# Kernel optimization log

Hardware: AMD Instinct MI355X
Metric: run time of the kernel (lower is better)

The kernel has to match this reference:

```python
import jax, jax.numpy as jnp
import numpy as np

H = 8
D = 64  # head_dim = node_dim // num_heads = 512 // 8
NODE = 512
EPS = 1e-5


def setup_inputs() -> dict:
    key = jax.random.key(0)
    ks = jax.random.split(key, 8)
    S, IN = 4096, 1024
    return {
        "protT5_emb": jax.random.normal(ks[0], (S, IN), jnp.float32),
        "contact_matrix": jax.random.uniform(ks[1], (S, S), jnp.float32),
        "Wq": jax.random.normal(ks[2], (NODE, IN), jnp.float32) * 0.02,
        "bq": jnp.zeros((NODE,), jnp.float32),
        "Wk": jax.random.normal(ks[3], (NODE, IN), jnp.float32) * 0.02,
        "bk": jnp.zeros((NODE,), jnp.float32),
        "Wv": jax.random.normal(ks[4], (NODE, IN), jnp.float32) * 0.02,
        "bv": jnp.zeros((NODE,), jnp.float32),
        "Wc": jnp.ones((1, H, 1, 1), jnp.float32),
        "Wo": jax.random.normal(ks[5], (NODE, NODE), jnp.float32) * 0.02,
        "bo": jnp.zeros((NODE,), jnp.float32),
        "gamma": jnp.ones((NODE,), jnp.float32),
        "beta": jnp.zeros((NODE,), jnp.float32),
    }


def reference(protT5_emb, contact_matrix, Wq, bq, Wk, bk, Wv, bv, Wc, Wo, bo, gamma, beta):
    S = protT5_emb.shape[0]
    # QKV projections -> [H, S, D]
    Q = (protT5_emb @ Wq.T + bq).reshape(S, H, D).transpose(1, 0, 2)
    K = (protT5_emb @ Wk.T + bk).reshape(S, H, D).transpose(1, 0, 2)
    V = (protT5_emb @ Wv.T + bv).reshape(S, H, D).transpose(1, 0, 2)
    # raw scores [H, S, S]
    attn_raw = jnp.einsum('hsd,htd->hst', Q, K) / jnp.sqrt(jnp.float32(D))
    # multiplicative contact mask, per-head learnable scale
    contact_mask = contact_matrix[None, :, :] * Wc.reshape(H, 1, 1)
    attn_weight = jax.nn.softmax(attn_raw * contact_mask, axis=-1)
    attn_output = jnp.einsum('hst,htd->hsd', attn_weight, V)  # [H, S, D]
    # FAITHFUL to torch: transpose(0,1).view(S,-1) on [1,H,S,D] flattens in
    # (head, seq, dim) order -> scrambled [S, H*D] reshape, not head concat.
    attn_output = attn_output.reshape(S, H * D)
    aug = attn_output @ Wo.T + bo
    x = aug + protT5_emb[:, :NODE]
    mu = jnp.mean(x, axis=-1, keepdims=True)
    var = jnp.mean((x - mu) ** 2, axis=-1, keepdims=True)
    return (x - mu) * jax.lax.rsqrt(var + EPS) * gamma + beta
```

## Files before the change

kernel.cpp:

```cpp
#include <hip/hip_runtime.h>
#include <stdint.h>

#define SEQ 4096
#define INDIM 1024
#define NODEDIM 512
#define NH 8
#define HD 64
#define LSTR 72

typedef __bf16 bf16x8 __attribute__((ext_vector_type(8)));
typedef float f32x4 __attribute__((ext_vector_type(4)));

#define GLOAD_LDS(gp, lp) \
    __builtin_amdgcn_global_load_lds( \
        (const __attribute__((address_space(1))) void*)(gp), \
        (__attribute__((address_space(3))) void*)(lp), 16, 0, 0)

__device__ __forceinline__ unsigned short f2bf(float f) {
    union { float f; uint32_t u; } v; v.f = f;
    uint32_t u = v.u;
    uint32_t r = (u + 0x7fffu + ((u >> 16) & 1u)) >> 16;
    return (unsigned short)r;
}

__device__ __forceinline__ float fast_exp2(float x) {
    float r;
    asm volatile("v_exp_f32 %0, %1" : "=v"(r) : "v"(x));
    return r;
}

__global__ __launch_bounds__(256) void cvt_all(const float* __restrict__ emb,
                                               const float* __restrict__ Wq,
                                               const float* __restrict__ Wk,
                                               const float* __restrict__ Wv,
                                               const float* __restrict__ Wo,
                                               unsigned short* __restrict__ demb,
                                               unsigned short* __restrict__ dwqkv,
                                               unsigned short* __restrict__ dwo) {
    int b = blockIdx.x;
    const float* src;
    unsigned short* dst;
    int off;
    if (b < 4096)      { src = emb; dst = demb;            off = b; }
    else if (b < 4608) { src = Wq;  dst = dwqkv;           off = b - 4096; }
    else if (b < 5120) { src = Wk;  dst = dwqkv + 524288;  off = b - 4608; }
    else if (b < 5632) { src = Wv;  dst = dwqkv + 1048576; off = b - 5120; }
    else               { src = Wo;  dst = dwo;             off = b - 5632; }
    int i = (off * 256 + threadIdx.x) * 4;
    float4 v = *(const float4*)(src + i);
    ushort4 o;
    o.x = f2bf(v.x); o.y = f2bf(v.y); o.z = f2bf(v.z); o.w = f2bf(v.w);
    *(ushort4*)(dst + i) = o;
}

__global__ __launch_bounds__(256) void qkv_gemm(const unsigned short* __restrict__ A,
                                                const unsigned short* __restrict__ B,
                                                const float* __restrict__ bq,
                                                const float* __restrict__ bk,
                                                const float* __restrict__ bv,
                                                unsigned short* __restrict__ Qo,
                                                unsigned short* __restrict__ Ko,
                                                unsigned short* __restrict__ VTo) {
    __shared__ unsigned short As[128 * 32];
    __shared__ unsigned short Bs[128 * 32];
    __shared__ unsigned short Ts[128 * 40];
    const int tid = threadIdx.x;
    const int lane = tid & 63, wave = tid >> 6;
    const int wm = wave >> 1, wn = wave & 1;
    const int quad = lane >> 4, l16 = lane & 15;
    const int m0 = blockIdx.x * 128;
    const int n0 = blockIdx.y * 128;

    const int srow = tid >> 2, sqq = tid & 3;

    f32x4 acc[4][4] = {};

    for (int k0 = 0; k0 < INDIM; k0 += 32) {
        __syncthreads();
        for (int i = 0; i < 2; ++i) {
            int row = srow + 64 * i;
            GLOAD_LDS(A + (size_t)(m0 + row) * INDIM + k0 + sqq * 8, &As[row * 32 + sqq * 8]);
            GLOAD_LDS(B + (size_t)(n0 + row) * INDIM + k0 + sqq * 8, &Bs[row * 32 + sqq * 8]);
        }
        __syncthreads();
        bf16x8 af[4], bf[4];
        for (int mi = 0; mi < 4; ++mi)
            af[mi] = *(const bf16x8*)&As[(wm * 64 + mi * 16 + l16) * 32 + quad * 8];
        for (int ni = 0; ni < 4; ++ni)
            bf[ni] = *(const bf16x8*)&Bs[(wn * 64 + ni * 16 + l16) * 32 + quad * 8];
        for (int mi = 0; mi < 4; ++mi)
            for (int ni = 0; ni < 4; ++ni)
                acc[mi][ni] = __builtin_amdgcn_mfma_f32_16x16x32_bf16(af[mi], bf[ni], acc[mi][ni], 0, 0, 0);
    }

    if (blockIdx.y < 8) {
        unsigned short* outp = (blockIdx.y < 4) ? Qo : Ko;
        const float* biasp = (blockIdx.y < 4) ? bq : bk;
        for (int mi = 0; mi < 4; ++mi)
            for (int ni = 0; ni < 4; ++ni)
                for (int r = 0; r < 4; ++r) {
                    int s = m0 + wm * 64 + mi * 16 + quad * 4 + r;
                    int n = n0 + wn * 64 + ni * 16 + l16;
                    int h = (n >> 6) & 7;
                    int dd = n & 63;
                    float v = acc[mi][ni][r] + biasp[n & 511];
                    outp[((size_t)h * SEQ + s) * HD + dd] = f2bf(v);
                }
    } else {
        for (int chunk = 0; chunk < 4; ++chunk) {
            const int cwm = chunk >> 1;
            const int milo = (chunk & 1) * 2;
            __syncthreads();
            if (wm == cwm) {
                for (int mi2 = 0; mi2 < 2; ++mi2) {
                    int mi = milo + mi2;
                    for (int ni = 0; ni < 4; ++ni) {
                        int ddf = wn * 64 + ni * 16 + l16;
                        float bias = bv[(n0 + ddf) & 511];
                        for (int r = 0; r < 4; ++r) {
                            int sl = mi2 * 16 + quad * 4 + r;
                            Ts[ddf * 40 + sl] = f2bf(acc[mi][ni][r] + bias);
                        }
                    }
                }
            }
            __syncthreads();
            for (int pass = 0; pass < 2; ++pass) {
                int c = pass * 256 + tid;
                int row = c >> 2, part = c & 3;
                int nfull = n0 + row;
                int h = (nfull >> 6) & 7, dd = nfull & 63;
                *(bf16x8*)(VTo + ((size_t)h * HD + dd) * SEQ + m0 + chunk * 32 + part * 8) =
                    *(const bf16x8*)&Ts[row * 40 + part * 8];
            }
        }
    }
}

__global__ __launch_bounds__(256, 4) void attn_kernel(const unsigned short* __restrict__ Q,
                                                      const unsigned short* __restrict__ K,
                                                      const unsigned short* __restrict__ VT,
                                                      const float* __restrict__ CM,
                                                      const float* __restrict__ Wc,
                                                      float* __restrict__ O0,
                                                      float* __restrict__ O1,
                                                      float* __restrict__ l0,
                                                      float* __restrict__ l1) {
    __shared__ unsigned short QPs[64 * LSTR];
    __shared__ unsigned short Ks[64 * LSTR];
    __shared__ unsigned short Vs[64 * LSTR];
    const int tid = threadIdx.x;
    const int lane = tid & 63, wave = tid >> 6;
    const int quad = lane >> 4, l16 = lane & 15;
    const int h = blockIdx.y;
    const int q0 = blockIdx.x * 64;
    const int split = blockIdx.z;
    float* __restrict__ Op = split ? O1 : O0;
    float* __restrict__ lp = split ? l1 : l0;
    const float wch = Wc[h] * 0.125f * 1.44269504f;

    const int srow0 = tid >> 3, spart = tid & 7;
    const int srow1 = (tid + 256) >> 3;

    {
        bf16x8 v0 = *(const bf16x8*)(Q + ((size_t)h * SEQ + q0 + srow0) * HD + spart * 8);
        bf16x8 v1 = *(const bf16x8*)(Q + ((size_t)h * SEQ + q0 + srow1) * HD + spart * 8);
        for (int j = 0; j < 8; ++j) {
            v0[j] = (__bf16)((float)v0[j] * wch);
            v1[j] = (__bf16)((float)v1[j] * wch);
        }
        *(bf16x8*)&QPs[srow0 * LSTR + spart * 8] = v0;
        *(bf16x8*)&QPs[srow1 * LSTR + spart * 8] = v1;
    }

    const int tbeg = split * (SEQ / 2);
    const int tend = tbeg + SEQ / 2;

    const unsigned short* kp0 = K + ((size_t)h * SEQ + tbeg + srow0) * HD + spart * 8;
    const unsigned short* kp1 = K + ((size_t)h * SEQ + tbeg + srow1) * HD + spart * 8;
    const unsigned short* vp0 = VT + ((size_t)h * HD + srow0) * SEQ + tbeg + spart * 8;
    const unsigned short* vp1 = VT + ((size_t)h * HD + srow1) * SEQ + tbeg + spart * 8;
    bf16x8 kr0 = *(const bf16x8*)kp0;
    bf16x8 kr1 = *(const bf16x8*)kp1;
    bf16x8 vr0 = *(const bf16x8*)vp0;
    bf16x8 vr1 = *(const bf16x8*)vp1;

    const float* cmbase = CM + (size_t)(q0 + wave * 16 + quad * 4) * SEQ + l16;
    float cmv[4][4];
    for (int r = 0; r < 4; ++r)
        for (int nt = 0; nt < 4; ++nt)
            cmv[r][nt] = cmbase[(size_t)r * SEQ + tbeg + nt * 16];

    __syncthreads();
    bf16x8 a0 = *(const bf16x8*)&QPs[(wave * 16 + l16) * LSTR + quad * 8];
    bf16x8 a1 = *(const bf16x8*)&QPs[(wave * 16 + l16) * LSTR + 32 + quad * 8];

    f32x4 O[4] = {};
    float l_part[4] = {0.f, 0.f, 0.f, 0.f};

    for (int t0 = tbeg; t0 < tend; t0 += 64) {
        __syncthreads();
        *(bf16x8*)&Ks[srow0 * LSTR + spart * 8] = kr0;
        *(bf16x8*)&Ks[srow1 * LSTR + spart * 8] = kr1;
        *(bf16x8*)&Vs[srow0 * LSTR + spart * 8] = vr0;
        *(bf16x8*)&Vs[srow1 * LSTR + spart * 8] = vr1;
        __syncthreads();

        float cmn[4][4];
        if (t0 + 64 < tend) {
            kr0 = *(const bf16x8*)(kp0 + (size_t)(t0 + 64 - tbeg) * HD);
            kr1 = *(const bf16x8*)(kp1 + (size_t)(t0 + 64 - tbeg) * HD);
            vr0 = *(const bf16x8*)(vp0 + (t0 + 64 - tbeg));
            vr1 = *(const bf16x8*)(vp1 + (t0 + 64 - tbeg));
            for (int r = 0; r < 4; ++r)
                for (int nt = 0; nt < 4; ++nt)
                    cmn[r][nt] = cmbase[(size_t)r * SEQ + t0 + 64 + nt * 16];
        }

        f32x4 sc[4];
        for (int nt = 0; nt < 4; ++nt) {
            bf16x8 b0 = *(const bf16x8*)&Ks[(nt * 16 + l16) * LSTR + quad * 8];
            bf16x8 b1 = *(const bf16x8*)&Ks[(nt * 16 + l16) * LSTR + 32 + quad * 8];
            f32x4 z = {0.f, 0.f, 0.f, 0.f};
            z = __builtin_amdgcn_mfma_f32_16x16x32_bf16(a0, b0, z, 0, 0, 0);
            z = __builtin_amdgcn_mfma_f32_16x16x32_bf16(a1, b1, z, 0, 0, 0);
            sc[nt] = z;
        }

        for (int r = 0; r < 4; ++r) {
            for (int nt = 0; nt < 4; ++nt) {
                float pv = fast_exp2(sc[nt][r] * cmv[r][nt]);
                l_part[r] += pv;
                union { float f; uint32_t u; } pu; pu.f = pv;
                QPs[(wave * 16 + quad * 4 + r) * LSTR + nt * 16 + l16] =
                    (unsigned short)(pu.u >> 16);
            }
        }

        for (int r = 0; r < 4; ++r)
            for (int nt = 0; nt < 4; ++nt)
                cmv[r][nt] = cmn[r][nt];

        asm volatile("s_waitcnt lgkmcnt(0)" ::: "memory");

        bf16x8 pa0 = *(const bf16x8*)&QPs[(wave * 16 + l16) * LSTR + quad * 8];
        bf16x8 pa1 = *(const bf16x8*)&QPs[(wave * 16 + l16) * LSTR + 32 + quad * 8];
        for (int nt = 0; nt < 4; ++nt) {
            bf16x8 vb0 = *(const bf16x8*)&Vs[(nt * 16 + l16) * LSTR + quad * 8];
            bf16x8 vb1 = *(const bf16x8*)&Vs[(nt * 16 + l16) * LSTR + 32 + quad * 8];
            f32x4 o = O[nt];
            o = __builtin_amdgcn_mfma_f32_16x16x32_bf16(pa0, vb0, o, 0, 0, 0);
            o = __builtin_amdgcn_mfma_f32_16x16x32_bf16(pa1, vb1, o, 0, 0, 0);
            O[nt] = o;
        }
    }

    for (int r = 0; r < 4; ++r) {
        float s = l_part[r];
        for (int off = 1; off < 16; off <<= 1) s += __shfl_xor(s, off);
        l_part[r] = s;
    }
    if (l16 == 0)
        for (int r = 0; r < 4; ++r)
            lp[(size_t)h * SEQ + q0 + wave * 16 + quad * 4 + r] = l_part[r];
    for (int nt = 0; nt < 4; ++nt)
        for (int r = 0; r < 4; ++r) {
            int sg = q0 + wave * 16 + quad * 4 + r;
            Op[((size_t)h * SEQ + sg) * HD + nt * 16 + l16] = O[nt][r];
        }
}

__global__ __launch_bounds__(256) void combine_kernel(const float* __restrict__ O0,
                                                      const float* __restrict__ O1,
                                                      const float* __restrict__ l0,
                                                      const float* __restrict__ l1,
                                                      unsigned short* __restrict__ AO) {
    int idx = blockIdx.x * 256 + threadIdx.x;
    int e = idx * 4;
    int row = e >> 6;
    float4 a = *(const float4*)(O0 + e);
    float4 b = *(const float4*)(O1 + e);
    float linv = 1.f / (l0[row] + l1[row]);
    ushort4 o;
    o.x = f2bf((a.x + b.x) * linv);
    o.y = f2bf((a.y + b.y) * linv);
    o.z = f2bf((a.z + b.z) * linv);
    o.w = f2bf((a.w + b.w) * linv);
    *(ushort4*)(AO + e) = o;
}

__global__ __launch_bounds__(256) void out_gemm(const unsigned short* __restrict__ A,
                                                const unsigned short* __restrict__ B,
                                                const float* __restrict__ bo,
                                                const float* __restrict__ emb,
                                                float* __restrict__ X) {
    __shared__ unsigned short As[64 * 32];
    __shared__ unsigned short Bs[128 * 32];
    const int tid = threadIdx.x;
    const int lane = tid & 63, wave = tid >> 6;
    const int quad = lane >> 4, l16 = lane & 15;
    const int m0 = blockIdx.x * 64;
    const int n0 = blockIdx.y * 128;

    const int srow = tid >> 2, sqq = tid & 3;

    f32x4 acc[8] = {};

    for (int k0 = 0; k0 < NODEDIM; k0 += 32) {
        __syncthreads();
        GLOAD_LDS(A + (size_t)(m0 + srow) * NODEDIM + k0 + sqq * 8, &As[srow * 32 + sqq * 8]);
        for (int i = 0; i < 2; ++i) {
            int row = srow + 64 * i;
            GLOAD_LDS(B + (size_t)(n0 + row) * NODEDIM + k0 + sqq * 8, &Bs[row * 32 + sqq * 8]);
        }
        __syncthreads();
        bf16x8 af = *(const bf16x8*)&As[(wave * 16 + l16) * 32 + quad * 8];
        for (int ni = 0; ni < 8; ++ni) {
            bf16x8 bf = *(const bf16x8*)&Bs[(ni * 16 + l16) * 32 + quad * 8];
            acc[ni] = __builtin_amdgcn_mfma_f32_16x16x32_bf16(af, bf, acc[ni], 0, 0, 0);
        }
    }

    for (int ni = 0; ni < 8; ++ni)
        for (int r = 0; r < 4; ++r) {
            int s = m0 + wave * 16 + quad * 4 + r;
            int n = n0 + ni * 16 + l16;
            float v = acc[ni][r] + bo[n] + emb[(size_t)s * INDIM + n];
            X[(size_t)s * NODEDIM + n] = v;
        }
}

__global__ __launch_bounds__(256) void ln_kernel(const float* __restrict__ X,
                                                 const float* __restrict__ gamma,
                                                 const float* __restrict__ beta,
                                                 float* __restrict__ out) {
    const int s = blockIdx.x;
    const int n = threadIdx.x * 2;
    float2 v = *(const float2*)&X[(size_t)s * NODEDIM + n];
    float sum = v.x + v.y;
    float sq = v.x * v.x + v.y * v.y;
    for (int off = 32; off > 0; off >>= 1) {
        sum += __shfl_down(sum, off);
        sq += __shfl_down(sq, off);
    }
    __shared__ float ssum[4], ssq[4];
    const int wave = threadIdx.x >> 6, lane = threadIdx.x & 63;
    if (lane == 0) { ssum[wave] = sum; ssq[wave] = sq; }
    __syncthreads();
    float tsum = ssum[0] + ssum[1] + ssum[2] + ssum[3];
    float tsq = ssq[0] + ssq[1] + ssq[2] + ssq[3];
    float mu = tsum * (1.f / 512.f);
    float var = tsq * (1.f / 512.f) - mu * mu;
    float rstd = rsqrtf(var + 1e-5f);
    float2 g = *(const float2*)&gamma[n];
    float2 b = *(const float2*)&beta[n];
    float2 o;
    o.x = (v.x - mu) * rstd * g.x + b.x;
    o.y = (v.y - mu) * rstd * g.y + b.y;
    *(float2*)&out[(size_t)s * NODEDIM + n] = o;
}

extern "C" void kernel_launch(void* const* d_in, const int* in_sizes, int n_in,
                              void* d_out, int out_size, void* d_ws, size_t ws_size,
                              hipStream_t stream) {
    const float* emb = (const float*)d_in[0];
    const float* cm  = (const float*)d_in[1];
    const float* Wq  = (const float*)d_in[2];
    const float* bq  = (const float*)d_in[3];
    const float* Wk  = (const float*)d_in[4];
    const float* bk  = (const float*)d_in[5];
    const float* Wv  = (const float*)d_in[6];
    const float* bv  = (const float*)d_in[7];
    const float* Wc  = (const float*)d_in[8];
    const float* Wo  = (const float*)d_in[9];
    const float* bo  = (const float*)d_in[10];
    const float* gamma = (const float*)d_in[11];
    const float* beta  = (const float*)d_in[12];
    float* out = (float*)d_out;

    unsigned short* ws = (unsigned short*)d_ws;
    unsigned short* emb_bf  = ws;
    unsigned short* wqkv_bf = emb_bf + 4194304;
    unsigned short* wo_bf   = wqkv_bf + 1572864;
    unsigned short* Qb  = wo_bf + 262144;
    unsigned short* Kb  = Qb + 2097152;
    unsigned short* VTb = Kb + 2097152;
    unsigned short* AOb = VTb + 2097152;
    float* X = (float*)(AOb + 2097152);
    float* O0 = (float*)emb_bf;
    float* O1 = X;
    float* l0 = (float*)wqkv_bf;
    float* l1 = l0 + NH * SEQ;

    cvt_all<<<5888, 256, 0, stream>>>(emb, Wq, Wk, Wv, Wo, emb_bf, wqkv_bf, wo_bf);

    qkv_gemm<<<dim3(32, 12), 256, 0, stream>>>(emb_bf, wqkv_bf, bq, bk, bv, Qb, Kb, VTb);
    attn_kernel<<<dim3(64, 8, 2), 256, 0, stream>>>(Qb, Kb, VTb, cm, Wc, O0, O1, l0, l1);
    combine_kernel<<<2048, 256, 0, stream>>>(O0, O1, l0, l1, AOb);
    out_gemm<<<dim3(64, 4), 256, 0, stream>>>(AOb, wo_bf, bo, emb, X);
    ln_kernel<<<4096, 256, 0, stream>>>(X, gamma, beta, out);
}
```

Measured before the change: 260.6 us.

## Fuse fp32-to-bf16 conversion into QKV and output GEMM tile loads

Removes the separate cvt_all pass. The QKV and output GEMMs now read fp32 inputs and weights directly and convert them to bf16 while staging into LDS. The QKV GEMM moves to a 128x64 per-head tile (768 blocks instead of 384), and the attention kernel loads its contact-mask values at the top of each iteration instead of prefetching them one step ahead. This saves one kernel launch and the bf16 round trip through memory, at the cost of twice the fp32 read bytes per GEMM tile, redundant conversion work across blocks, and synchronous loads in place of async LDS loads.

```diff
diff --git a/kernel.cpp b/kernel.cpp
--- a/kernel.cpp
+++ b/kernel.cpp
@@ -29,32 +29,20 @@
     return r;
 }
 
-__global__ __launch_bounds__(256) void cvt_all(const float* __restrict__ emb,
-                                               const float* __restrict__ Wq,
-                                               const float* __restrict__ Wk,
-                                               const float* __restrict__ Wv,
-                                               const float* __restrict__ Wo,
-                                               unsigned short* __restrict__ demb,
-                                               unsigned short* __restrict__ dwqkv,
-                                               unsigned short* __restrict__ dwo) {
-    int b = blockIdx.x;
-    const float* src;
-    unsigned short* dst;
-    int off;
-    if (b < 4096)      { src = emb; dst = demb;            off = b; }
-    else if (b < 4608) { src = Wq;  dst = dwqkv;           off = b - 4096; }
-    else if (b < 5120) { src = Wk;  dst = dwqkv + 524288;  off = b - 4608; }
-    else if (b < 5632) { src = Wv;  dst = dwqkv + 1048576; off = b - 5120; }
-    else               { src = Wo;  dst = dwo;             off = b - 5632; }
-    int i = (off * 256 + threadIdx.x) * 4;
-    float4 v = *(const float4*)(src + i);
-    ushort4 o;
-    o.x = f2bf(v.x); o.y = f2bf(v.y); o.z = f2bf(v.z); o.w = f2bf(v.w);
-    *(ushort4*)(dst + i) = o;
-}
-
-__global__ __launch_bounds__(256) void qkv_gemm(const unsigned short* __restrict__ A,
-                                                const unsigned short* __restrict__ B,
+__device__ __forceinline__ void cvt8(const float* __restrict__ p, unsigned short* dst) {
+    float4 u = *(const float4*)p;
+    float4 w = *(const float4*)(p + 4);
+    ushort4 a, b;
+    a.x = f2bf(u.x); a.y = f2bf(u.y); a.z = f2bf(u.z); a.w = f2bf(u.w);
+    b.x = f2bf(w.x); b.y = f2bf(w.y); b.z = f2bf(w.z); b.w = f2bf(w.w);
+    *(ushort4*)dst = a;
+    *(ushort4*)(dst + 4) = b;
+}
+
+__global__ __launch_bounds__(256) void qkv_gemm(const float* __restrict__ emb,
+                                                const float* __restrict__ Wq,
+                                                const float* __restrict__ Wk,
+                                                const float* __restrict__ Wv,
                                                 const float* __restrict__ bq,
                                                 const float* __restrict__ bk,
                                                 const float* __restrict__ bv,
@@ -62,77 +50,74 @@
                                                 unsigned short* __restrict__ Ko,
                                                 unsigned short* __restrict__ VTo) {
     __shared__ unsigned short As[128 * 32];
-    __shared__ unsigned short Bs[128 * 32];
-    __shared__ unsigned short Ts[128 * 40];
+    __shared__ unsigned short Bs[64 * 32];
+    __shared__ unsigned short Ts[64 * 40];
     const int tid = threadIdx.x;
     const int lane = tid & 63, wave = tid >> 6;
-    const int wm = wave >> 1, wn = wave & 1;
     const int quad = lane >> 4, l16 = lane & 15;
     const int m0 = blockIdx.x * 128;
-    const int n0 = blockIdx.y * 128;
-
-    const int srow = tid >> 2, sqq = tid & 3;
-
-    f32x4 acc[4][4] = {};
+    const int role = blockIdx.y >> 3;
+    const int h = blockIdx.y & 7;
+    const int n0 = h * 64;
+    const float* __restrict__ Wsrc = (role == 0) ? Wq : (role == 1) ? Wk : Wv;
+    const float* __restrict__ bias = (role == 0) ? bq : (role == 1) ? bk : bv;
+
+    f32x4 acc[2][4] = {};
 
     for (int k0 = 0; k0 < INDIM; k0 += 32) {
         __syncthreads();
         for (int i = 0; i < 2; ++i) {
-            int row = srow + 64 * i;
-            GLOAD_LDS(A + (size_t)(m0 + row) * INDIM + k0 + sqq * 8, &As[row * 32 + sqq * 8]);
-            GLOAD_LDS(B + (size_t)(n0 + row) * INDIM + k0 + sqq * 8, &Bs[row * 32 + sqq * 8]);
-        }
-        __syncthreads();
-        bf16x8 af[4], bf[4];
-        for (int mi = 0; mi < 4; ++mi)
-            af[mi] = *(const bf16x8*)&As[(wm * 64 + mi * 16 + l16) * 32 + quad * 8];
+            int c = tid + 256 * i;
+            int row = c >> 2, seg = c & 3;
+            unsigned short tmp[8];
+            cvt8(emb + (size_t)(m0 + row) * INDIM + k0 + seg * 8, tmp);
+            *(bf16x8*)&As[row * 32 + seg * 8] = *(bf16x8*)tmp;
+        }
+        {
+            int row = tid >> 2, seg = tid & 3;
+            unsigned short tmp[8];
+            cvt8(Wsrc + (size_t)(n0 + row) * INDIM + k0 + seg * 8, tmp);
+            *(bf16x8*)&Bs[row * 32 + seg * 8] = *(bf16x8*)tmp;
+        }
+        __syncthreads();
+        bf16x8 af[2], bf[4];
+        for (int mi = 0; mi < 2; ++mi)
+            af[mi] = *(const bf16x8*)&As[(wave * 32 + mi * 16 + l16) * 32 + quad * 8];
         for (int ni = 0; ni < 4; ++ni)
-            bf[ni] = *(const bf16x8*)&Bs[(wn * 64 + ni * 16 + l16) * 32 + quad * 8];
-        for (int mi = 0; mi < 4; ++mi)
+            bf[ni] = *(const bf16x8*)&Bs[(ni * 16 + l16) * 32 + quad * 8];
+        for (int mi = 0; mi < 2; ++mi)
             for (int ni = 0; ni < 4; ++ni)
                 acc[mi][ni] = __builtin_amdgcn_mfma_f32_16x16x32_bf16(af[mi], bf[ni], acc[mi][ni], 0, 0, 0);
     }
 
-    if (blockIdx.y < 8) {
-        unsigned short* outp = (blockIdx.y < 4) ? Qo : Ko;
-        const float* biasp = (blockIdx.y < 4) ? bq : bk;
-        for (int mi = 0; mi < 4; ++mi)
+    if (role < 2) {
+        unsigned short* outp = (role == 0) ? Qo : Ko;
+        for (int mi = 0; mi < 2; ++mi)
             for (int ni = 0; ni < 4; ++ni)
                 for (int r = 0; r < 4; ++r) {
-                    int s = m0 + wm * 64 + mi * 16 + quad * 4 + r;
-                    int n = n0 + wn * 64 + ni * 16 + l16;
-                    int h = (n >> 6) & 7;
-                    int dd = n & 63;
-                    float v = acc[mi][ni][r] + biasp[n & 511];
+                    int s = m0 + wave * 32 + mi * 16 + quad * 4 + r;
+                    int dd = ni * 16 + l16;
+                    float v = acc[mi][ni][r] + bias[n0 + dd];
                     outp[((size_t)h * SEQ + s) * HD + dd] = f2bf(v);
                 }
     } else {
         for (int chunk = 0; chunk < 4; ++chunk) {
-            const int cwm = chunk >> 1;
-            const int milo = (chunk & 1) * 2;
             __syncthreads();
-            if (wm == cwm) {
-                for (int mi2 = 0; mi2 < 2; ++mi2) {
-                    int mi = milo + mi2;
+            if (wave == chunk) {
+                for (int mi = 0; mi < 2; ++mi)
                     for (int ni = 0; ni < 4; ++ni) {
-                        int ddf = wn * 64 + ni * 16 + l16;
-                        float bias = bv[(n0 + ddf) & 511];
+                        int ddf = ni * 16 + l16;
+                        float bv_ = bias[n0 + ddf];
                         for (int r = 0; r < 4; ++r) {
-                            int sl = mi2 * 16 + quad * 4 + r;
-                            Ts[ddf * 40 + sl] = f2bf(acc[mi][ni][r] + bias);
+                            int sl = mi * 16 + quad * 4 + r;
+                            Ts[ddf * 40 + sl] = f2bf(acc[mi][ni][r] + bv_);
                         }
                     }
-                }
             }
             __syncthreads();
-            for (int pass = 0; pass < 2; ++pass) {
-                int c = pass * 256 + tid;
-                int row = c >> 2, part = c & 3;
-                int nfull = n0 + row;
-                int h = (nfull >> 6) & 7, dd = nfull & 63;
-                *(bf16x8*)(VTo + ((size_t)h * HD + dd) * SEQ + m0 + chunk * 32 + part * 8) =
-                    *(const bf16x8*)&Ts[row * 40 + part * 8];
-            }
+            int row = tid >> 2, part = tid & 3;
+            *(bf16x8*)(VTo + ((size_t)h * HD + row) * SEQ + m0 + chunk * 32 + part * 8) =
+                *(const bf16x8*)&Ts[row * 40 + part * 8];
         }
     }
 }
@@ -185,20 +170,20 @@
     bf16x8 vr0 = *(const bf16x8*)vp0;
     bf16x8 vr1 = *(const bf16x8*)vp1;
 
-    const float* cmbase = CM + (size_t)(q0 + wave * 16 + quad * 4) * SEQ + l16;
-    float cmv[4][4];
-    for (int r = 0; r < 4; ++r)
-        for (int nt = 0; nt < 4; ++nt)
-            cmv[r][nt] = cmbase[(size_t)r * SEQ + tbeg + nt * 16];
-
     __syncthreads();
     bf16x8 a0 = *(const bf16x8*)&QPs[(wave * 16 + l16) * LSTR + quad * 8];
     bf16x8 a1 = *(const bf16x8*)&QPs[(wave * 16 + l16) * LSTR + 32 + quad * 8];
 
     f32x4 O[4] = {};
     float l_part[4] = {0.f, 0.f, 0.f, 0.f};
+    const float* cmbase = CM + (size_t)(q0 + wave * 16 + quad * 4) * SEQ + l16;
 
     for (int t0 = tbeg; t0 < tend; t0 += 64) {
+        float cmv[4][4];
+        for (int r = 0; r < 4; ++r)
+            for (int nt = 0; nt < 4; ++nt)
+                cmv[r][nt] = cmbase[(size_t)r * SEQ + t0 + nt * 16];
+
         __syncthreads();
         *(bf16x8*)&Ks[srow0 * LSTR + spart * 8] = kr0;
         *(bf16x8*)&Ks[srow1 * LSTR + spart * 8] = kr1;
@@ -206,15 +191,11 @@
         *(bf16x8*)&Vs[srow1 * LSTR + spart * 8] = vr1;
         __syncthreads();
 
-        float cmn[4][4];
         if (t0 + 64 < tend) {
             kr0 = *(const bf16x8*)(kp0 + (size_t)(t0 + 64 - tbeg) * HD);
             kr1 = *(const bf16x8*)(kp1 + (size_t)(t0 + 64 - tbeg) * HD);
             vr0 = *(const bf16x8*)(vp0 + (t0 + 64 - tbeg));
             vr1 = *(const bf16x8*)(vp1 + (t0 + 64 - tbeg));
-            for (int r = 0; r < 4; ++r)
-                for (int nt = 0; nt < 4; ++nt)
-                    cmn[r][nt] = cmbase[(size_t)r * SEQ + t0 + 64 + nt * 16];
         }
 
         f32x4 sc[4];
@@ -236,10 +217,6 @@
                     (unsigned short)(pu.u >> 16);
             }
         }
-
-        for (int r = 0; r < 4; ++r)
-            for (int nt = 0; nt < 4; ++nt)
-                cmv[r][nt] = cmn[r][nt];
 
         asm volatile("s_waitcnt lgkmcnt(0)" ::: "memory");
 
@@ -290,7 +267,7 @@
 }
 
 __global__ __launch_bounds__(256) void out_gemm(const unsigned short* __restrict__ A,
-                                                const unsigned short* __restrict__ B,
+                                                const float* __restrict__ Wo,
                                                 const float* __restrict__ bo,
                                                 const float* __restrict__ emb,
                                                 float* __restrict__ X) {
@@ -310,8 +287,11 @@
         __syncthreads();
         GLOAD_LDS(A + (size_t)(m0 + srow) * NODEDIM + k0 + sqq * 8, &As[srow * 32 + sqq * 8]);
         for (int i = 0; i < 2; ++i) {
-            int row = srow + 64 * i;
-            GLOAD_LDS(B + (size_t)(n0 + row) * NODEDIM + k0 + sqq * 8, &Bs[row * 32 + sqq * 8]);
+            int c = tid + 256 * i;
+            int row = c >> 2, seg = c & 3;
+            unsigned short tmp[8];
+            cvt8(Wo + (size_t)(n0 + row) * NODEDIM + k0 + seg * 8, tmp);
+            *(bf16x8*)&Bs[row * 32 + seg * 8] = *(bf16x8*)tmp;
         }
         __syncthreads();
         bf16x8 af = *(const bf16x8*)&As[(wave * 16 + l16) * 32 + quad * 8];
@@ -379,24 +359,19 @@
     float* out = (float*)d_out;
 
     unsigned short* ws = (unsigned short*)d_ws;
-    unsigned short* emb_bf  = ws;
-    unsigned short* wqkv_bf = emb_bf + 4194304;
-    unsigned short* wo_bf   = wqkv_bf + 1572864;
-    unsigned short* Qb  = wo_bf + 262144;
+    float* O0 = (float*)ws;
+    float* l0 = (float*)(ws + 4194304);
+    float* l1 = l0 + NH * SEQ;
+    unsigned short* Qb  = ws + 4325376;
     unsigned short* Kb  = Qb + 2097152;
     unsigned short* VTb = Kb + 2097152;
     unsigned short* AOb = VTb + 2097152;
     float* X = (float*)(AOb + 2097152);
-    float* O0 = (float*)emb_bf;
     float* O1 = X;
-    float* l0 = (float*)wqkv_bf;
-    float* l1 = l0 + NH * SEQ;
-
-    cvt_all<<<5888, 256, 0, stream>>>(emb, Wq, Wk, Wv, Wo, emb_bf, wqkv_bf, wo_bf);
-
-    qkv_gemm<<<dim3(32, 12), 256, 0, stream>>>(emb_bf, wqkv_bf, bq, bk, bv, Qb, Kb, VTb);
+
+    qkv_gemm<<<dim3(32, 24), 256, 0, stream>>>(emb, Wq, Wk, Wv, bq, bk, bv, Qb, Kb, VTb);
     attn_kernel<<<dim3(64, 8, 2), 256, 0, stream>>>(Qb, Kb, VTb, cm, Wc, O0, O1, l0, l1);
     combine_kernel<<<2048, 256, 0, stream>>>(O0, O1, l0, l1, AOb);
-    out_gemm<<<dim3(64, 4), 256, 0, stream>>>(AOb, wo_bf, bo, emb, X);
+    out_gemm<<<dim3(64, 4), 256, 0, stream>>>(AOb, Wo, bo, emb, X);
     ln_kernel<<<4096, 256, 0, stream>>>(X, gamma, beta, out);
 }
```

New measurement: 276.6 us. 1.06x slower.

## Double query rows per attention block to reuse K/V tiles across two M-tiles

Applied to the files above, without the earlier changes.

Each attention block now handles 128 query rows instead of 64, and each wave computes two 16-row M-tiles against every K/V tile it stages in LDS. This halves how often K and V are reloaded per query and halves the grid to 512 blocks. The contact-matrix prefetch into registers for the next tile is dropped, so those loads are now issued at the top of each iteration and their latency is no longer hidden by the previous tile's work. Register pressure roughly doubles for the accumulators, which may lower occupancy with only 512 blocks.

```diff
diff --git a/kernel.cpp b/kernel.cpp
--- a/kernel.cpp
+++ b/kernel.cpp
@@ -146,36 +146,32 @@
                                                       float* __restrict__ O1,
                                                       float* __restrict__ l0,
                                                       float* __restrict__ l1) {
-    __shared__ unsigned short QPs[64 * LSTR];
+    __shared__ unsigned short QPs[128 * LSTR];
     __shared__ unsigned short Ks[64 * LSTR];
     __shared__ unsigned short Vs[64 * LSTR];
     const int tid = threadIdx.x;
     const int lane = tid & 63, wave = tid >> 6;
     const int quad = lane >> 4, l16 = lane & 15;
     const int h = blockIdx.y;
-    const int q0 = blockIdx.x * 64;
+    const int q0 = blockIdx.x * 128;
     const int split = blockIdx.z;
     float* __restrict__ Op = split ? O1 : O0;
     float* __restrict__ lp = split ? l1 : l0;
     const float wch = Wc[h] * 0.125f * 1.44269504f;
 
+    for (int i = 0; i < 4; ++i) {
+        int c = tid + 256 * i;
+        int row = c >> 3, part = c & 7;
+        bf16x8 v = *(const bf16x8*)(Q + ((size_t)h * SEQ + q0 + row) * HD + part * 8);
+        for (int j = 0; j < 8; ++j) v[j] = (__bf16)((float)v[j] * wch);
+        *(bf16x8*)&QPs[row * LSTR + part * 8] = v;
+    }
+
+    const int tbeg = split * (SEQ / 2);
+    const int tend = tbeg + SEQ / 2;
+
     const int srow0 = tid >> 3, spart = tid & 7;
     const int srow1 = (tid + 256) >> 3;
-
-    {
-        bf16x8 v0 = *(const bf16x8*)(Q + ((size_t)h * SEQ + q0 + srow0) * HD + spart * 8);
-        bf16x8 v1 = *(const bf16x8*)(Q + ((size_t)h * SEQ + q0 + srow1) * HD + spart * 8);
-        for (int j = 0; j < 8; ++j) {
-            v0[j] = (__bf16)((float)v0[j] * wch);
-            v1[j] = (__bf16)((float)v1[j] * wch);
-        }
-        *(bf16x8*)&QPs[srow0 * LSTR + spart * 8] = v0;
-        *(bf16x8*)&QPs[srow1 * LSTR + spart * 8] = v1;
-    }
-
-    const int tbeg = split * (SEQ / 2);
-    const int tend = tbeg + SEQ / 2;
-
     const unsigned short* kp0 = K + ((size_t)h * SEQ + tbeg + srow0) * HD + spart * 8;
     const unsigned short* kp1 = K + ((size_t)h * SEQ + tbeg + srow1) * HD + spart * 8;
     const unsigned short* vp0 = VT + ((size_t)h * HD + srow0) * SEQ + tbeg + spart * 8;
@@ -185,20 +181,26 @@
     bf16x8 vr0 = *(const bf16x8*)vp0;
     bf16x8 vr1 = *(const bf16x8*)vp1;
 
-    const float* cmbase = CM + (size_t)(q0 + wave * 16 + quad * 4) * SEQ + l16;
-    float cmv[4][4];
-    for (int r = 0; r < 4; ++r)
-        for (int nt = 0; nt < 4; ++nt)
-            cmv[r][nt] = cmbase[(size_t)r * SEQ + tbeg + nt * 16];
-
     __syncthreads();
-    bf16x8 a0 = *(const bf16x8*)&QPs[(wave * 16 + l16) * LSTR + quad * 8];
-    bf16x8 a1 = *(const bf16x8*)&QPs[(wave * 16 + l16) * LSTR + 32 + quad * 8];
-
-    f32x4 O[4] = {};
-    float l_part[4] = {0.f, 0.f, 0.f, 0.f};
+    bf16x8 a[2][2];
+    for (int mi = 0; mi < 2; ++mi) {
+        a[mi][0] = *(const bf16x8*)&QPs[(wave * 32 + mi * 16 + l16) * LSTR + quad * 8];
+        a[mi][1] = *(const bf16x8*)&QPs[(wave * 32 + mi * 16 + l16) * LSTR + 32 + quad * 8];
+    }
+
+    f32x4 O[2][4] = {};
+    float l_part[2][4] = {};
+    const float* cmbase0 = CM + (size_t)(q0 + wave * 32 + quad * 4) * SEQ + l16;
+    const float* cmbase1 = cmbase0 + (size_t)16 * SEQ;
 
     for (int t0 = tbeg; t0 < tend; t0 += 64) {
+        float cmv[2][4][4];
+        for (int r = 0; r < 4; ++r)
+            for (int nt = 0; nt < 4; ++nt) {
+                cmv[0][r][nt] = cmbase0[(size_t)r * SEQ + t0 + nt * 16];
+                cmv[1][r][nt] = cmbase1[(size_t)r * SEQ + t0 + nt * 16];
+            }
+
         __syncthreads();
         *(bf16x8*)&Ks[srow0 * LSTR + spart * 8] = kr0;
         *(bf16x8*)&Ks[srow1 * LSTR + spart * 8] = kr1;
@@ -206,68 +208,70 @@
         *(bf16x8*)&Vs[srow1 * LSTR + spart * 8] = vr1;
         __syncthreads();
 
-        float cmn[4][4];
         if (t0 + 64 < tend) {
             kr0 = *(const bf16x8*)(kp0 + (size_t)(t0 + 64 - tbeg) * HD);
             kr1 = *(const bf16x8*)(kp1 + (size_t)(t0 + 64 - tbeg) * HD);
             vr0 = *(const bf16x8*)(vp0 + (t0 + 64 - tbeg));
             vr1 = *(const bf16x8*)(vp1 + (t0 + 64 - tbeg));
-            for (int r = 0; r < 4; ++r)
-                for (int nt = 0; nt < 4; ++nt)
-                    cmn[r][nt] = cmbase[(size_t)r * SEQ + t0 + 64 + nt * 16];
-        }
-
-        f32x4 sc[4];
+        }
+
+        f32x4 sc[2][4];
         for (int nt = 0; nt < 4; ++nt) {
             bf16x8 b0 = *(const bf16x8*)&Ks[(nt * 16 + l16) * LSTR + quad * 8];
             bf16x8 b1 = *(const bf16x8*)&Ks[(nt * 16 + l16) * LSTR + 32 + quad * 8];
-            f32x4 z = {0.f, 0.f, 0.f, 0.f};
-            z = __builtin_amdgcn_mfma_f32_16x16x32_bf16(a0, b0, z, 0, 0, 0);
-            z = __builtin_amdgcn_mfma_f32_16x16x32_bf16(a1, b1, z, 0, 0, 0);
-            sc[nt] = z;
-        }
-
-        for (int r = 0; r < 4; ++r) {
-            for (int nt = 0; nt < 4; ++nt) {
-                float pv = fast_exp2(sc[nt][r] * cmv[r][nt]);
-                l_part[r] += pv;
-                union { float f; uint32_t u; } pu; pu.f = pv;
-                QPs[(wave * 16 + quad * 4 + r) * LSTR + nt * 16 + l16] =
-                    (unsigned short)(pu.u >> 16);
-            }
-        }
-
-        for (int r = 0; r < 4; ++r)
-            for (int nt = 0; nt < 4; ++nt)
-                cmv[r][nt] = cmn[r][nt];
+            for (int mi = 0; mi < 2; ++mi) {
+                f32x4 z = {0.f, 0.f, 0.f, 0.f};
+                z = __builtin_amdgcn_mfma_f32_16x16x32_bf16(a[mi][0], b0, z, 0, 0, 0);
+                z = __builtin_amdgcn_mfma_f32_16x16x32_bf16(a[mi][1], b1, z, 0, 0, 0);
+                sc[mi][nt] = z;
+            }
+        }
+
+        for (int mi = 0; mi < 2; ++mi)
+            for (int r = 0; r < 4; ++r)
+                for (int nt = 0; nt < 4; ++nt) {
+                    float pv = fast_exp2(sc[mi][nt][r] * cmv[mi][r][nt]);
+                    l_part[mi][r] += pv;
+                    union { float f; uint32_t u; } pu; pu.f = pv;
+                    QPs[(wave * 32 + mi * 16 + quad * 4 + r) * LSTR + nt * 16 + l16] =
+                        (unsigned short)(pu.u >> 16);
+                }
 
         asm volatile("s_waitcnt lgkmcnt(0)" ::: "memory");
 
-        bf16x8 pa0 = *(const bf16x8*)&QPs[(wave * 16 + l16) * LSTR + quad * 8];
-        bf16x8 pa1 = *(const bf16x8*)&QPs[(wave * 16 + l16) * LSTR + 32 + quad * 8];
+        bf16x8 pa[2][2];
+        for (int mi = 0; mi < 2; ++mi) {
+            pa[mi][0] = *(const bf16x8*)&QPs[(wave * 32 + mi * 16 + l16) * LSTR + quad * 8];
+            pa[mi][1] = *(const bf16x8*)&QPs[(wave * 32 + mi * 16 + l16) * LSTR + 32 + quad * 8];
+        }
         for (int nt = 0; nt < 4; ++nt) {
             bf16x8 vb0 = *(const bf16x8*)&Vs[(nt * 16 + l16) * LSTR + quad * 8];
             bf16x8 vb1 = *(const bf16x8*)&Vs[(nt * 16 + l16) * LSTR + 32 + quad * 8];
-            f32x4 o = O[nt];
-            o = __builtin_amdgcn_mfma_f32_16x16x32_bf16(pa0, vb0, o, 0, 0, 0);
-            o = __builtin_amdgcn_mfma_f32_16x16x32_bf16(pa1, vb1, o, 0, 0, 0);
-            O[nt] = o;
-        }
-    }
-
-    for (int r = 0; r < 4; ++r) {
-        float s = l_part[r];
-        for (int off = 1; off < 16; off <<= 1) s += __shfl_xor(s, off);
-        l_part[r] = s;
-    }
+            for (int mi = 0; mi < 2; ++mi) {
+                f32x4 o = O[mi][nt];
+                o = __builtin_amdgcn_mfma_f32_16x16x32_bf16(pa[mi][0], vb0, o, 0, 0, 0);
+                o = __builtin_amdgcn_mfma_f32_16x16x32_bf16(pa[mi][1], vb1, o, 0, 0, 0);
+                O[mi][nt] = o;
+            }
+        }
+    }
+
+    for (int mi = 0; mi < 2; ++mi)
+        for (int r = 0; r < 4; ++r) {
+            float s = l_part[mi][r];
+            for (int off = 1; off < 16; off <<= 1) s += __shfl_xor(s, off);
+            l_part[mi][r] = s;
+        }
     if (l16 == 0)
-        for (int r = 0; r < 4; ++r)
-            lp[(size_t)h * SEQ + q0 + wave * 16 + quad * 4 + r] = l_part[r];
-    for (int nt = 0; nt < 4; ++nt)
-        for (int r = 0; r < 4; ++r) {
-            int sg = q0 + wave * 16 + quad * 4 + r;
-            Op[((size_t)h * SEQ + sg) * HD + nt * 16 + l16] = O[nt][r];
-        }
+        for (int mi = 0; mi < 2; ++mi)
+            for (int r = 0; r < 4; ++r)
+                lp[(size_t)h * SEQ + q0 + wave * 32 + mi * 16 + quad * 4 + r] = l_part[mi][r];
+    for (int mi = 0; mi < 2; ++mi)
+        for (int nt = 0; nt < 4; ++nt)
+            for (int r = 0; r < 4; ++r) {
+                int sg = q0 + wave * 32 + mi * 16 + quad * 4 + r;
+                Op[((size_t)h * SEQ + sg) * HD + nt * 16 + l16] = O[mi][nt][r];
+            }
 }
 
 __global__ __launch_bounds__(256) void combine_kernel(const float* __restrict__ O0,
@@ -395,7 +399,7 @@
     cvt_all<<<5888, 256, 0, stream>>>(emb, Wq, Wk, Wv, Wo, emb_bf, wqkv_bf, wo_bf);
 
     qkv_gemm<<<dim3(32, 12), 256, 0, stream>>>(emb_bf, wqkv_bf, bq, bk, bv, Qb, Kb, VTb);
-    attn_kernel<<<dim3(64, 8, 2), 256, 0, stream>>>(Qb, Kb, VTb, cm, Wc, O0, O1, l0, l1);
+    attn_kernel<<<dim3(32, 8, 2), 256, 0, stream>>>(Qb, Kb, VTb, cm, Wc, O0, O1, l0, l1);
     combine_kernel<<<2048, 256, 0, stream>>>(O0, O1, l0, l1, AOb);
     out_gemm<<<dim3(64, 4), 256, 0, stream>>>(AOb, wo_bf, bo, emb, X);
     ln_kernel<<<4096, 256, 0, stream>>>(X, gamma, beta, out);
```

Result: slower. 368.4 us (+41.4%).
